# Kernel optimization log

Measured on AMD Instinct MI355X. Metric: run time of the kernel, lower is better.

## Reference

```python
import math
import jax, jax.numpy as jnp
import numpy as np

T, B, E, H = 2048, 1, 2048, 32
HD = E // H          # head_dim = 64
HALF = HD // 2       # rotary half = 32
SCALE_LENGTH = 1024


def duplicate_interleave(m):
    # [S, HALF] -> [S, HD], each column duplicated adjacently
    return jnp.repeat(m, 2, axis=-1)


def rotate_every_two(x):
    # x: [BH, S, HD]
    x1 = x[:, :, ::2]
    x2 = x[:, :, 1::2]
    return jnp.stack((-x2, x1), axis=-1).reshape(x.shape)


def apply_rotary_pos_emb(x, sin, cos, scale):
    # sin/cos/scale: [S, HALF]; x: [BH, S, HD]
    sin2 = duplicate_interleave(sin * scale)
    cos2 = duplicate_interleave(cos * scale)
    return x * cos2 + rotate_every_two(x) * sin2


def setup_inputs() -> dict:
    key = jax.random.key(0)
    ks = jax.random.split(key, 8)
    std = 0.02
    query = jax.random.normal(ks[0], (T, B, E), jnp.float32)
    key_t = jax.random.normal(ks[1], (T, B, E), jnp.float32)
    value = jax.random.normal(ks[2], (T, B, E), jnp.float32)
    Wq = jax.random.normal(ks[3], (E, E), jnp.float32) * std
    Wk = jax.random.normal(ks[4], (E, E), jnp.float32) * std
    Wv = jax.random.normal(ks[5], (E, E), jnp.float32) * std
    Wo = jax.random.normal(ks[6], (E, E), jnp.float32) * std
    bq = jnp.zeros((E,), jnp.float32)
    bk = jnp.zeros((E,), jnp.float32)
    bv = jnp.zeros((E,), jnp.float32)
    bo = jnp.zeros((E,), jnp.float32)
    # XPos-style rotary tables
    pos = jnp.arange(T, dtype=jnp.float32)
    inv_freq = 1.0 / (10000.0 ** (jnp.arange(HALF, dtype=jnp.float32) / HALF))
    ang = pos[:, None] * inv_freq[None, :]          # [T, HALF]
    sin = jnp.sin(ang)
    cos = jnp.cos(ang)
    scale_base = 512.0
    dim_scale = (jnp.arange(0, HD, 2, dtype=jnp.float32) + 0.4 * HD) / (1.4 * HD)
    xscale = dim_scale[None, :] ** (pos[:, None] / scale_base)  # [T, HALF]
    # causal additive mask
    attn_mask = jnp.where(jnp.triu(jnp.ones((T, T), bool), k=1), -1e9, 0.0).astype(jnp.float32)
    return {"query": query, "key": key_t, "value": value,
            "Wq": Wq, "bq": bq, "Wk": Wk, "bk": bk, "Wv": Wv, "bv": bv,
            "Wo": Wo, "bo": bo, "sin": sin, "cos": cos, "xscale": xscale,
            "attn_mask": attn_mask, "scale_length": SCALE_LENGTH}


def reference(query, key, value, Wq, bq, Wk, bk, Wv, bv, Wo, bo,
              sin, cos, xscale, attn_mask, scale_length):
    tgt_len, bsz, embed_dim = query.shape
    scaling = HD ** -0.5

    def proj(x, W, b):
        y = x @ W.T + b                                # [T, B, E]
        return y.reshape(tgt_len, bsz * H, HD).transpose(1, 0, 2)  # [BH, T, HD]

    q = proj(query, Wq, bq)
    k = proj(key, Wk, bk)
    v = proj(value, Wv, bv)

    # self-attention XPos rotary: k scaled by 1/xscale, q by xscale (last q_len rows)
    k = apply_rotary_pos_emb(k, sin, cos, 1.0 / xscale)
    q = apply_rotary_pos_emb(q, sin[-tgt_len:], cos[-tgt_len:], xscale[-tgt_len:])

    src_len = k.shape[1]
    if src_len > scale_length:
        pos_k = jnp.arange(src_len - tgt_len, src_len, dtype=jnp.float32)
        scale_attention = jnp.maximum(1.0, jnp.log(pos_k) / math.log(scale_length))
        q = q * scale_attention[None, :, None]

    q = q * scaling
    attn_weights = jnp.einsum('btd,bsd->bts', q, k)      # [BH, T, S]
    attn_weights = attn_weights + attn_mask[None, :, :]
    attn_weights = jax.nn.softmax(attn_weights.astype(jnp.float32), axis=-1
                                  ).astype(q.dtype)
    attn = jnp.einsum('bts,bsd->btd', attn_weights, v)   # [BH, T, HD]
    attn = attn.transpose(1, 0, 2).reshape(tgt_len, bsz, embed_dim)
    attn = attn @ Wo.T + bo
    return attn
```

## Files before the change

### kernel.cpp

```cpp
#include <hip/hip_runtime.h>
#include <hip/hip_bf16.h>
#include <math.h>

#define T_LEN 2048
#define EMB   2048
#define NH    32
#define HD    64
#define HALF  32

typedef __attribute__((ext_vector_type(8))) short short8v;
typedef __attribute__((ext_vector_type(4))) float floatx4;

__device__ inline void gload_lds16(const void* g, void* l) {
    __builtin_amdgcn_global_load_lds(
        (const __attribute__((address_space(1))) unsigned int*)g,
        (__attribute__((address_space(3))) unsigned int*)l,
        16, 0, 0);
}

__device__ inline ushort f2bf(float x) {
    union { float f; unsigned u; } c; c.f = x;
    const unsigned r = c.u + 0x7FFFu + ((c.u >> 16) & 1u);
    return (ushort)(r >> 16);
}

#define BARRIER() do { asm volatile("" ::: "memory"); \
    __builtin_amdgcn_s_barrier(); asm volatile("" ::: "memory"); } while (0)
#define VMW8() asm volatile("s_waitcnt vmcnt(8)" ::: "memory")
#define VMW0() asm volatile("s_waitcnt vmcnt(0)" ::: "memory")

__global__ __launch_bounds__(256) void conv_all(
    const float* __restrict__ s0, const float* __restrict__ s1,
    const float* __restrict__ s2, const float* __restrict__ s3,
    const float* __restrict__ s4, const float* __restrict__ s5,
    const float* __restrict__ s6, ushort* __restrict__ dst,
    const float* __restrict__ sinp, const float* __restrict__ cosp,
    const float* __restrict__ xscale,
    float2* __restrict__ qt, float2* __restrict__ kt)
{
    if (blockIdx.x >= 14336) {
        const int idx = (blockIdx.x - 14336) * 256 + threadIdx.x;
        const int t = idx >> 5;
        const float s = sinp[idx], c = cosp[idx], xs = xscale[idx];
        float sa = 1.f;
        if (t >= 2) {
            const float lv = __logf((float)t) * 0.14426950408889634f;
            sa = lv > 1.f ? lv : 1.f;
        }
        const float qs = xs * sa * 0.125f * 1.4426950408889634f;
        qt[idx] = make_float2(c * qs, s * qs);
        const float ks = 1.f / xs;
        kt[idx] = make_float2(c * ks, s * ks);
        return;
    }
    const int idx = blockIdx.x * 256 + threadIdx.x;
    const int t = idx >> 19;
    const int r = (idx & 524287) * 8;
    const float* in = t == 0 ? s0 : t == 1 ? s1 : t == 2 ? s2 : t == 3 ? s3
                    : t == 4 ? s4 : t == 5 ? s5 : s6;
    const float4 v0 = *reinterpret_cast<const float4*>(&in[r]);
    const float4 v1 = *reinterpret_cast<const float4*>(&in[r + 4]);
    ushort o[8];
    o[0] = f2bf(v0.x); o[1] = f2bf(v0.y); o[2] = f2bf(v0.z); o[3] = f2bf(v0.w);
    o[4] = f2bf(v1.x); o[5] = f2bf(v1.y); o[6] = f2bf(v1.z); o[7] = f2bf(v1.w);
    *reinterpret_cast<uint4*>(&dst[(size_t)t * 4194304 + r]) =
        *reinterpret_cast<const uint4*>(o);
}

#define QBM 256
#define QBN 256

#define STAGE_A3(tau, h, slot) do {                                            \
    const int _tc = (tau) * 64;                                                \
    _Pragma("unroll") for (int _i = 0; _i < 2; ++_i) {                         \
        gload_lds16(&Ap[(size_t)(bm + (h) * 128 + wid * 16 + _i * 8 + rl) * 2048 + _tc + csw], \
                    &lds[(slot) * 16384 + (h) * 8192 + (wid * 16 + _i * 8) * 64]); \
    } } while (0)

#define STAGE_B2(tau, h, slot) do {                                            \
    const int _tc = (tau) * 64;                                                \
    _Pragma("unroll") for (int _i = 0; _i < 2; ++_i) {                         \
        gload_lds16(&Bp[(size_t)(bn + (h) * 128 + wid * 16 + _i * 8 + rl) * 2048 + _tc + csw], \
                    &lds[49152 + (slot) * 16384 + (h) * 8192 + (wid * 16 + _i * 8) * 64]); \
    } } while (0)

#define PH(sa_, sb_, mp, VMWSTMT, PREBAR, ENDBAR, ...) do {                    \
    if ((mp) == 0) {                                                           \
        _Pragma("unroll") for (int n = 0; n < 4; ++n) {                        \
            bf[n][0] = ldB(sb_, n, 0);                                         \
            bf[n][1] = ldB(sb_, n, 1);                                         \
        }                                                                      \
    }                                                                          \
    af[0][0] = ldA(sa_, (mp) * 2, 0);     af[0][1] = ldA(sa_, (mp) * 2, 1);    \
    af[1][0] = ldA(sa_, (mp) * 2 + 1, 0); af[1][1] = ldA(sa_, (mp) * 2 + 1, 1);\
    __VA_ARGS__;                                                               \
    PREBAR;                                                                    \
    __builtin_amdgcn_s_setprio(1);                                             \
    _Pragma("unroll") for (int mm = 0; mm < 2; ++mm)                           \
    _Pragma("unroll") for (int n = 0; n < 4; ++n)                              \
    _Pragma("unroll") for (int kk = 0; kk < 2; ++kk)                           \
        acc[(mp) * 2 + mm][n] = __builtin_amdgcn_mfma_f32_16x16x32_bf16(       \
            af[mm][kk], bf[n][kk], acc[(mp) * 2 + mm][n], 0, 0, 0);            \
    __builtin_amdgcn_s_setprio(0);                                             \
    VMWSTMT;                                                                   \
    ENDBAR;                                                                    \
} while (0)

#define TILE6(sa, sb, sa2, tau2, LASTVMW) do {                                 \
    PH(sa, sb, 0, (void)0, (void)0,   (void)0,   STAGE_A3(tau2, 0, sa2));      \
    PH(sa, sb, 1, (void)0, BARRIER(), (void)0,   STAGE_A3(tau2, 1, sa2));      \
    PH(sa, sb, 2, (void)0, (void)0,   (void)0,   STAGE_B2(tau2, 0, sb));       \
    PH(sa, sb, 3, LASTVMW, (void)0,   BARRIER(), STAGE_B2(tau2, 1, sb));       \
} while (0)

__global__ __launch_bounds__(512, 2) void gemm_qkv8(
    const ushort* __restrict__ Astack,
    const ushort* __restrict__ Wstack,
    const float* __restrict__ bq, const float* __restrict__ bk,
    const float* __restrict__ bv,
    ushort* __restrict__ outQ, ushort* __restrict__ outK,
    ushort* __restrict__ outVt,
    const float2* __restrict__ qtab, const float2* __restrict__ ktab)
{
    __shared__ ushort lds[81920];
    const int tid  = threadIdx.x;
    const int lane = tid & 63;
    const int wid  = tid >> 6;

    const int b   = blockIdx.x + blockIdx.y * 24;
    const int xcd = b & 7;
    const int idx = b >> 3;
    const int bx  = xcd * 3 + (idx >> 3);
    const int by  = idx & 7;
    const int which = bx >> 3;
    const int bn  = (bx & 7) * QBN;
    const int bm  = by * QBM;
    const ushort* Ap = Astack + (size_t)which * 4194304;
    const ushort* Bp = Wstack + (size_t)which * 4194304;

    const int rl  = lane >> 3;
    const int csw = (((lane & 7) ^ ((lane >> 3) & 7)) * 8);
    const int lm  = lane & 15;
    const int lg  = lane >> 4;
    const char* ldsb = reinterpret_cast<const char*>(lds);

    auto ldA = [&](int slot, int m, int kk) -> short8v {
        const int row = m * 16 + lm;
        const int off = (slot * 16384 + (wid >> 2) * 8192) * 2 + row * 128
                      + (((kk * 4 + lg) ^ (row & 7)) * 16);
        return *reinterpret_cast<const short8v*>(ldsb + off);
    };
    auto ldB = [&](int slot, int n, int kk) -> short8v {
        const int row = (wid & 1) * 64 + n * 16 + lm;
        const int off = (49152 + slot * 16384 + ((wid & 3) >> 1) * 8192) * 2
                      + row * 128 + (((kk * 4 + lg) ^ (row & 7)) * 16);
        return *reinterpret_cast<const short8v*>(ldsb + off);
    };

    floatx4 acc[8][4] = {};
    short8v bf[4][2];
    short8v af[2][2];

    STAGE_A3(0, 0, 0); STAGE_A3(0, 1, 0);
    STAGE_B2(0, 0, 0); STAGE_B2(0, 1, 0);
    STAGE_A3(1, 0, 1); STAGE_A3(1, 1, 1);
    STAGE_B2(1, 0, 1); STAGE_B2(1, 1, 1);
    VMW8();
    BARRIER();

    for (int i = 0; i < 5; ++i) {
        const int t = 6 * i;
        TILE6(0, 0, 2, t + 2, VMW8());
        TILE6(1, 1, 0, t + 3, VMW8());
        TILE6(2, 0, 1, t + 4, VMW8());
        TILE6(0, 1, 2, t + 5, VMW8());
        TILE6(1, 0, 0, t + 6, VMW8());
        TILE6(2, 1, 1, t + 7, VMW8());
    }
    PH(0, 0, 0, (void)0, (void)0,   (void)0,   (void)0);
    PH(0, 0, 1, (void)0, (void)0,   (void)0,   (void)0);
    PH(0, 0, 2, (void)0, (void)0,   (void)0,   (void)0);
    PH(0, 0, 3, VMW0(),  (void)0,   BARRIER(), (void)0);
    PH(1, 1, 0, (void)0, (void)0, (void)0, (void)0);
    PH(1, 1, 1, (void)0, (void)0, (void)0, (void)0);
    PH(1, 1, 2, (void)0, (void)0, (void)0, (void)0);
    PH(1, 1, 3, (void)0, (void)0, (void)0, (void)0);

    const float* bias = which == 0 ? bq : which == 1 ? bk : bv;
    const float2* tbl = which == 0 ? qtab : ktab;
    #pragma unroll
    for (int m = 0; m < 8; ++m) {
        #pragma unroll
        for (int n = 0; n < 4; ++n) {
            const int col = bn + (wid & 3) * 64 + n * 16 + lm;
            const float bz = bias[col];
            const int row0 = bm + (wid >> 2) * 128 + m * 16 + lg * 4;
            if (which == 2) {
                ushort o4[4];
                #pragma unroll
                for (int j = 0; j < 4; ++j)
                    o4[j] = f2bf(acc[m][n][j] + bz);
                *reinterpret_cast<uint2*>(&outVt[(size_t)col * T_LEN + row0]) =
                    *reinterpret_cast<const uint2*>(o4);
            } else {
                ushort* O = which == 0 ? outQ : outK;
                const int p = (col & 63) >> 1;
                const bool even = (col & 1) == 0;
                #pragma unroll
                for (int j = 0; j < 4; ++j) {
                    const int row = row0 + j;
                    const float v = acc[m][n][j] + bz;
                    const float pv = __shfl_xor(v, 1);
                    const float2 cs = tbl[row * HALF + p];
                    const float outv = even ? v * cs.x - pv * cs.y
                                            : v * cs.x + pv * cs.y;
                    O[(size_t)row * EMB + col] = f2bf(outv);
                }
            }
        }
    }
}

#define GBM 128
#define GBN 128
#define GBK 64

__global__ __launch_bounds__(256) void gemm_out_sk(
    const ushort* __restrict__ A,
    const ushort* __restrict__ B,
    ushort* __restrict__ P)
{
    __shared__ ushort As[GBM * GBK];
    __shared__ ushort Bs[GBN * GBK];
    const int tid  = threadIdx.x;
    const int lane = tid & 63;
    const int wid  = tid >> 6;
    const int bm = blockIdx.y * GBM;
    const int bn = blockIdx.x * GBN;
    const int z  = blockIdx.z;
    const int wr = (wid >> 1) * 64;
    const int wc = (wid & 1) * 64;

    floatx4 acc[4][4] = {};

    const int lrow  = lane >> 3;
    const int lcolb = (lane & 7) * 8;

    for (int k0 = z * 1024; k0 < (z + 1) * 1024; k0 += GBK) {
        #pragma unroll
        for (int c = 0; c < 4; ++c) {
            const int chunk = wid * 4 + c;
            const int row = chunk * 8 + lrow;
            gload_lds16(&A[(size_t)(bm + row) * EMB + k0 + lcolb], &As[chunk * 512]);
            gload_lds16(&B[(size_t)(bn + row) * EMB + k0 + lcolb], &Bs[chunk * 512]);
        }
        __syncthreads();
        #pragma unroll
        for (int kk = 0; kk < 2; ++kk) {
            short8v a[4], b[4];
            #pragma unroll
            for (int m = 0; m < 4; ++m)
                a[m] = *reinterpret_cast<const short8v*>(
                    &As[(wr + m * 16 + (lane & 15)) * GBK + kk * 32 + (lane >> 4) * 8]);
            #pragma unroll
            for (int n = 0; n < 4; ++n)
                b[n] = *reinterpret_cast<const short8v*>(
                    &Bs[(wc + n * 16 + (lane & 15)) * GBK + kk * 32 + (lane >> 4) * 8]);
            #pragma unroll
            for (int m = 0; m < 4; ++m)
                #pragma unroll
                for (int n = 0; n < 4; ++n)
                    acc[m][n] = __builtin_amdgcn_mfma_f32_16x16x32_bf16(
                        a[m], b[n], acc[m][n], 0, 0, 0);
        }
        __syncthreads();
    }

    ushort* Pz = P + (size_t)z * 4194304;
    const int cr = (lane >> 4) * 4;
    const int cc = lane & 15;
    #pragma unroll
    for (int m = 0; m < 4; ++m) {
        #pragma unroll
        for (int n = 0; n < 4; ++n) {
            const int col = bn + wc + n * 16 + cc;
            #pragma unroll
            for (int j = 0; j < 4; ++j) {
                const int row = bm + wr + m * 16 + cr + j;
                Pz[(size_t)row * EMB + col] = f2bf(acc[m][n][j]);
            }
        }
    }
}

__global__ __launch_bounds__(256) void reduce_out(
    const ushort* __restrict__ P, const float* __restrict__ bias,
    float* __restrict__ C)
{
    const int i = (blockIdx.x * 256 + threadIdx.x) * 8;
    const uint4 pa = *reinterpret_cast<const uint4*>(&P[i]);
    const uint4 pb = *reinterpret_cast<const uint4*>(&P[4194304 + i]);
    const ushort* ua = reinterpret_cast<const ushort*>(&pa);
    const ushort* ub = reinterpret_cast<const ushort*>(&pb);
    const int cb = i & 2047;
    float o[8];
    #pragma unroll
    for (int j = 0; j < 8; ++j) {
        union { unsigned u; float f; } fa, fb;
        fa.u = (unsigned)ua[j] << 16;
        fb.u = (unsigned)ub[j] << 16;
        o[j] = fa.f + fb.f + bias[cb + j];
    }
    *reinterpret_cast<float4*>(&C[i])     = make_float4(o[0], o[1], o[2], o[3]);
    *reinterpret_cast<float4*>(&C[i + 4]) = make_float4(o[4], o[5], o[6], o[7]);
}

__global__ __launch_bounds__(256) void flash_attn_mfma(
    const ushort* __restrict__ Qb,
    const ushort* __restrict__ Kb,
    const ushort* __restrict__ Vt,
    ushort* __restrict__ Ob)
{
    __shared__ ushort Ks[2][64 * 64];
    __shared__ ushort Vs[2][64 * 64];
    __shared__ ushort Ps[4][16 * 64];

    const int h   = blockIdx.x;
    const int qb  = (T_LEN / 64 - 1) - blockIdx.y;
    const int tid = threadIdx.x;
    const int lane = tid & 63;
    const int wid  = tid >> 6;
    const int qrow_w = qb * 64 + wid * 16;
    const int lm = lane & 15;
    const int lg = lane >> 4;

    short8v qf[2];
    {
        const ushort* qp = &Qb[(size_t)(qrow_w + lm) * EMB + h * HD + lg * 8];
        qf[0] = *reinterpret_cast<const short8v*>(qp);
        qf[1] = *reinterpret_cast<const short8v*>(qp + 32);
    }

    floatx4 oacc[4] = {};
    float m = -1e30f, l = 0.f;

    const int srow = lane >> 3;
    const int schk = lane & 7;

    {
        #pragma unroll
        for (int i = 0; i < 2; ++i) {
            const int slot = wid * 2 + i;
            const int row  = slot * 8 + srow;
            const int cswz = (schk ^ (row & 7)) * 8;
            gload_lds16(&Kb[(size_t)row * EMB + h * HD + cswz], &Ks[0][slot * 512]);
            gload_lds16(&Vt[(size_t)(h * HD + row) * T_LEN + cswz], &Vs[0][slot * 512]);
        }
    }
    __syncthreads();

    for (int kb = 0; kb <= qb; ++kb) {
        const int cur = kb & 1;
        if (kb < qb) {
            const int nkb = kb + 1;
            #pragma unroll
            for (int i = 0; i < 2; ++i) {
                const int slot = wid * 2 + i;
                const int row  = slot * 8 + srow;
                const int cswz = (schk ^ (row & 7)) * 8;
                gload_lds16(&Kb[(size_t)(nkb * 64 + row) * EMB + h * HD + cswz],
                            &Ks[cur ^ 1][slot * 512]);
                gload_lds16(&Vt[(size_t)(h * HD + row) * T_LEN + nkb * 64 + cswz],
                            &Vs[cur ^ 1][slot * 512]);
            }
        }

        float sv[16];
        __builtin_amdgcn_s_setprio(1);
        #pragma unroll
        for (int t = 0; t < 4; ++t) {
            floatx4 sacc = {};
            const int srow_l = t * 16 + lm;
            const char* krow = reinterpret_cast<const char*>(Ks[cur]) + srow_l * 128;
            const int swz = (srow_l & 7) << 4;
            #pragma unroll
            for (int kk = 0; kk < 2; ++kk) {
                const int cb = (kk * 64 + lg * 16) ^ swz;
                short8v kf = *reinterpret_cast<const short8v*>(krow + cb);
                sacc = __builtin_amdgcn_mfma_f32_16x16x32_bf16(kf, qf[kk], sacc, 0, 0, 0);
            }
            sv[t * 4 + 0] = sacc[0]; sv[t * 4 + 1] = sacc[1];
            sv[t * 4 + 2] = sacc[2]; sv[t * 4 + 3] = sacc[3];
        }
        __builtin_amdgcn_s_setprio(0);

        const int qg = qrow_w + lm;
        if (kb == qb) {
            #pragma unroll
            for (int t = 0; t < 4; ++t)
                #pragma unroll
                for (int r = 0; r < 4; ++r) {
                    const int sg = kb * 64 + t * 16 + lg * 4 + r;
                    if (sg > qg) sv[t * 4 + r] = -1e30f;
                }
        }

        const float mx0 = fmaxf(fmaxf(fmaxf(sv[0], sv[1]), fmaxf(sv[2], sv[3])),
                                fmaxf(fmaxf(sv[4], sv[5]), fmaxf(sv[6], sv[7])));
        const float mx1 = fmaxf(fmaxf(fmaxf(sv[8], sv[9]), fmaxf(sv[10], sv[11])),
                                fmaxf(fmaxf(sv[12], sv[13]), fmaxf(sv[14], sv[15])));
        float mx = fmaxf(mx0, mx1);
        mx = fmaxf(mx, __shfl_xor(mx, 16));
        mx = fmaxf(mx, __shfl_xor(mx, 32));
        float corr = 1.f;
        if (!__all(mx - m <= 11.544f)) {
            const float mnew = fmaxf(m, mx);
            corr = exp2f(m - mnew);
            m = mnew;
            float corr4[4];
            #pragma unroll
            for (int r = 0; r < 4; ++r)
                corr4[r] = __shfl(corr, lg * 4 + r);
            #pragma unroll
            for (int td = 0; td < 4; ++td)
                #pragma unroll
                for (int r = 0; r < 4; ++r)
                    oacc[td][r] *= corr4[r];
        }
        float psum[8];
        unsigned pw[8];
        #pragma unroll
        for (int i = 0; i < 8; ++i) {
            const float p0 = exp2f(sv[2 * i + 0] - m);
            const float p1 = exp2f(sv[2 * i + 1] - m);
            psum[i] = p0 + p1;
            const __hip_bfloat162 h2 = __float22bfloat162_rn(make_float2(p0, p1));
            pw[i] = *reinterpret_cast<const unsigned*>(&h2);
        }
        float ps = ((psum[0] + psum[1]) + (psum[2] + psum[3]))
                 + ((psum[4] + psum[5]) + (psum[6] + psum[7]));
        ps += __shfl_xor(ps, 16);
        ps += __shfl_xor(ps, 32);
        l = l * corr + ps;

        {
            char* pbase = reinterpret_cast<char*>(&Ps[wid][0]) + lm * 128;
            const int swz = (lm & 7) << 4;
            #pragma unroll
            for (int t = 0; t < 4; ++t) {
                uint2 w;
                w.x = pw[2 * t + 0];
                w.y = pw[2 * t + 1];
                const int cb = (t * 32 + lg * 8) ^ swz;
                *reinterpret_cast<uint2*>(pbase + cb) = w;
            }
        }

        const char* pwave = reinterpret_cast<const char*>(&Ps[wid][0]);
        __builtin_amdgcn_s_setprio(1);
        #pragma unroll
        for (int kk = 0; kk < 2; ++kk) {
            const int acb = (kk * 64 + lg * 16) ^ ((lm & 7) << 4);
            short8v pa = *reinterpret_cast<const short8v*>(pwave + lm * 128 + acb);
            #pragma unroll
            for (int td = 0; td < 4; ++td) {
                const int d = td * 16 + lm;
                const int bcb = (kk * 64 + lg * 16) ^ ((d & 7) << 4);
                short8v vb = *reinterpret_cast<const short8v*>(
                    reinterpret_cast<const char*>(Vs[cur]) + d * 128 + bcb);
                oacc[td] = __builtin_amdgcn_mfma_f32_16x16x32_bf16(pa, vb, oacc[td], 0, 0, 0);
            }
        }
        __builtin_amdgcn_s_setprio(0);

        __syncthreads();
    }

    float invl[4];
    #pragma unroll
    for (int r = 0; r < 4; ++r)
        invl[r] = 1.f / __shfl(l, lg * 4 + r);
    #pragma unroll
    for (int td = 0; td < 4; ++td) {
        #pragma unroll
        for (int r = 0; r < 4; ++r) {
            const int trow = qrow_w + lg * 4 + r;
            const int col  = h * HD + td * 16 + lm;
            Ob[(size_t)trow * EMB + col] = f2bf(oacc[td][r] * invl[r]);
        }
    }
}

extern "C" void kernel_launch(void* const* d_in, const int* in_sizes, int n_in,
                              void* d_out, int out_size, void* d_ws, size_t ws_size,
                              hipStream_t stream) {
    const float* query = (const float*)d_in[0];
    const float* key   = (const float*)d_in[1];
    const float* value = (const float*)d_in[2];
    const float* Wq = (const float*)d_in[3];
    const float* bq = (const float*)d_in[4];
    const float* Wk = (const float*)d_in[5];
    const float* bk = (const float*)d_in[6];
    const float* Wv = (const float*)d_in[7];
    const float* bv = (const float*)d_in[8];
    const float* Wo = (const float*)d_in[9];
    const float* bo = (const float*)d_in[10];
    const float* sinp   = (const float*)d_in[11];
    const float* cosp   = (const float*)d_in[12];
    const float* xscale = (const float*)d_in[13];
    float* out = (float*)d_out;

    const size_t MB = 1024 * 1024;
    char* ws = (char*)d_ws;
    ushort* bWqkv = (ushort*)(ws + 0 * MB);
    ushort* bWo   = (ushort*)(ws + 24 * MB);
    ushort* bAqkv = (ushort*)(ws + 32 * MB);
    ushort* bQ  = (ushort*)(ws + 56 * MB);
    ushort* bK  = (ushort*)(ws + 64 * MB);
    ushort* bVt = (ushort*)(ws + 72 * MB);
    ushort* bAo = (ushort*)(ws + 80 * MB);
    float2* qtab = (float2*)(ws + 88 * MB);
    float2* ktab = (float2*)(ws + 88 * MB + 512 * 1024);
    ushort* Pout = (ushort*)(ws + 32 * MB);

    conv_all<<<14336 + 256, 256, 0, stream>>>(
        Wq, Wk, Wv, Wo, query, key, value, bWqkv,
        sinp, cosp, xscale, qtab, ktab);

    dim3 gQKV(24, 8);
    gemm_qkv8<<<gQKV, 512, 0, stream>>>(bAqkv, bWqkv, bq, bk, bv,
                                        bQ, bK, bVt, qtab, ktab);

    dim3 gFlash(NH, T_LEN / 64);
    flash_attn_mfma<<<gFlash, 256, 0, stream>>>(bQ, bK, bVt, bAo);

    dim3 gOut(EMB / GBN, T_LEN / GBM, 2);
    gemm_out_sk<<<gOut, 256, 0, stream>>>(bAo, bWo, Pout);
    reduce_out<<<T_LEN * EMB / (256 * 8), 256, 0, stream>>>(Pout, bo, out);
}
```

Measured before the change: 167.6 us.

## Fuse fp32-to-bf16 activation conversion into the QKV GEMM A-tile staging

The separate conversion pass for query/key/value activations is removed. The QKV GEMM now loads fp32 A tiles into registers, packs them to bf16 and writes them to swizzled LDS itself, with a reworked software pipeline and waitcnt schedule. This saves writing and re-reading 24MB of bf16 activations. In exchange it doubles the GEMM's global A traffic, raises register pressure, and the A loads no longer use direct-to-LDS transfers.

Result: slower. 268.2 us (+60.1%).

```diff
diff --git a/kernel.cpp b/kernel.cpp
--- a/kernel.cpp
+++ b/kernel.cpp
@@ -24,22 +24,30 @@
     return (ushort)(r >> 16);
 }
 
+__device__ inline unsigned pk2bf(float a, float b) {
+    __hip_bfloat162 h2 = __float22bfloat162_rn(make_float2(a, b));
+    return *reinterpret_cast<unsigned*>(&h2);
+}
+
 #define BARRIER() do { asm volatile("" ::: "memory"); \
     __builtin_amdgcn_s_barrier(); asm volatile("" ::: "memory"); } while (0)
-#define VMW8() asm volatile("s_waitcnt vmcnt(8)" ::: "memory")
-#define VMW0() asm volatile("s_waitcnt vmcnt(0)" ::: "memory")
+#define VMW16() asm volatile("s_waitcnt vmcnt(16)" ::: "memory")
+#define VMW12() asm volatile("s_waitcnt vmcnt(12)" ::: "memory")
+#define VMW8()  asm volatile("s_waitcnt vmcnt(8)"  ::: "memory")
+#define VMW4()  asm volatile("s_waitcnt vmcnt(4)"  ::: "memory")
+#define VMW0()  asm volatile("s_waitcnt vmcnt(0)"  ::: "memory")
+#define LGKM0() asm volatile("s_waitcnt lgkmcnt(0)" ::: "memory")
 
 __global__ __launch_bounds__(256) void conv_all(
     const float* __restrict__ s0, const float* __restrict__ s1,
     const float* __restrict__ s2, const float* __restrict__ s3,
-    const float* __restrict__ s4, const float* __restrict__ s5,
-    const float* __restrict__ s6, ushort* __restrict__ dst,
+    ushort* __restrict__ dst,
     const float* __restrict__ sinp, const float* __restrict__ cosp,
     const float* __restrict__ xscale,
     float2* __restrict__ qt, float2* __restrict__ kt)
 {
-    if (blockIdx.x >= 14336) {
-        const int idx = (blockIdx.x - 14336) * 256 + threadIdx.x;
+    if (blockIdx.x >= 8192) {
+        const int idx = (blockIdx.x - 8192) * 256 + threadIdx.x;
         const int t = idx >> 5;
         const float s = sinp[idx], c = cosp[idx], xs = xscale[idx];
         float sa = 1.f;
@@ -56,8 +64,7 @@
     const int idx = blockIdx.x * 256 + threadIdx.x;
     const int t = idx >> 19;
     const int r = (idx & 524287) * 8;
-    const float* in = t == 0 ? s0 : t == 1 ? s1 : t == 2 ? s2 : t == 3 ? s3
-                    : t == 4 ? s4 : t == 5 ? s5 : s6;
+    const float* in = t == 0 ? s0 : t == 1 ? s1 : t == 2 ? s2 : s3;
     const float4 v0 = *reinterpret_cast<const float4*>(&in[r]);
     const float4 v1 = *reinterpret_cast<const float4*>(&in[r + 4]);
     ushort o[8];
@@ -70,13 +77,6 @@
 #define QBM 256
 #define QBN 256
 
-#define STAGE_A3(tau, h, slot) do {                                            \
-    const int _tc = (tau) * 64;                                                \
-    _Pragma("unroll") for (int _i = 0; _i < 2; ++_i) {                         \
-        gload_lds16(&Ap[(size_t)(bm + (h) * 128 + wid * 16 + _i * 8 + rl) * 2048 + _tc + csw], \
-                    &lds[(slot) * 16384 + (h) * 8192 + (wid * 16 + _i * 8) * 64]); \
-    } } while (0)
-
 #define STAGE_B2(tau, h, slot) do {                                            \
     const int _tc = (tau) * 64;                                                \
     _Pragma("unroll") for (int _i = 0; _i < 2; ++_i) {                         \
@@ -84,17 +84,37 @@
                     &lds[49152 + (slot) * 16384 + (h) * 8192 + (wid * 16 + _i * 8) * 64]); \
     } } while (0)
 
-#define PH(sa_, sb_, mp, VMWSTMT, PREBAR, ENDBAR, ...) do {                    \
-    if ((mp) == 0) {                                                           \
-        _Pragma("unroll") for (int n = 0; n < 4; ++n) {                        \
-            bf[n][0] = ldB(sb_, n, 0);                                         \
-            bf[n][1] = ldB(sb_, n, 1);                                         \
-        }                                                                      \
-    }                                                                          \
+#define LOAD_A(tau, h) do {                                                    \
+    _Pragma("unroll") for (int _i = 0; _i < 2; ++_i) {                         \
+        const float* _s = &Af[(size_t)(bm + (h) * 128 + wid * 16 + _i * 8 + rl) * 2048 \
+                              + (tau) * 64 + (lane & 7) * 8];                  \
+        arA[h][_i] = *reinterpret_cast<const float4*>(_s);                     \
+        arB[h][_i] = *reinterpret_cast<const float4*>(_s + 4);                 \
+    } } while (0)
+
+#define WRITE_A(h, slot) do {                                                  \
+    _Pragma("unroll") for (int _i = 0; _i < 2; ++_i) {                         \
+        uint4 _v;                                                              \
+        _v.x = pk2bf(arA[h][_i].x, arA[h][_i].y);                              \
+        _v.y = pk2bf(arA[h][_i].z, arA[h][_i].w);                              \
+        _v.z = pk2bf(arB[h][_i].x, arB[h][_i].y);                              \
+        _v.w = pk2bf(arB[h][_i].z, arB[h][_i].w);                              \
+        *reinterpret_cast<uint4*>(ldsw + (slot) * 32768 + (h) * 16384          \
+            + (wid * 16 + _i * 8 + rl) * 128 + (((lane & 7) ^ rl) * 16)) = _v; \
+    } } while (0)
+
+#define RDB(sb_) do {                                                          \
+    _Pragma("unroll") for (int n = 0; n < 4; ++n) {                            \
+        bf[n][0] = ldB(sb_, n, 0);                                             \
+        bf[n][1] = ldB(sb_, n, 1);                                             \
+    } } while (0)
+
+#define RDA(sa_, mp) do {                                                      \
     af[0][0] = ldA(sa_, (mp) * 2, 0);     af[0][1] = ldA(sa_, (mp) * 2, 1);    \
     af[1][0] = ldA(sa_, (mp) * 2 + 1, 0); af[1][1] = ldA(sa_, (mp) * 2 + 1, 1);\
-    __VA_ARGS__;                                                               \
-    PREBAR;                                                                    \
+    } while (0)
+
+#define MFMA(mp) do {                                                          \
     __builtin_amdgcn_s_setprio(1);                                             \
     _Pragma("unroll") for (int mm = 0; mm < 2; ++mm)                           \
     _Pragma("unroll") for (int n = 0; n < 4; ++n)                              \
@@ -102,19 +122,19 @@
         acc[(mp) * 2 + mm][n] = __builtin_amdgcn_mfma_f32_16x16x32_bf16(       \
             af[mm][kk], bf[n][kk], acc[(mp) * 2 + mm][n], 0, 0, 0);            \
     __builtin_amdgcn_s_setprio(0);                                             \
-    VMWSTMT;                                                                   \
-    ENDBAR;                                                                    \
 } while (0)
 
-#define TILE6(sa, sb, sa2, tau2, LASTVMW) do {                                 \
-    PH(sa, sb, 0, (void)0, (void)0,   (void)0,   STAGE_A3(tau2, 0, sa2));      \
-    PH(sa, sb, 1, (void)0, BARRIER(), (void)0,   STAGE_A3(tau2, 1, sa2));      \
-    PH(sa, sb, 2, (void)0, (void)0,   (void)0,   STAGE_B2(tau2, 0, sb));       \
-    PH(sa, sb, 3, LASTVMW, (void)0,   BARRIER(), STAGE_B2(tau2, 1, sb));       \
+#define TILE6F(saR, saW, sb, tau2) do {                                        \
+    RDB(sb); RDA(saR, 0); VMW8(); WRITE_A(0, saW); LOAD_A(tau2, 0); MFMA(0);   \
+    RDA(saR, 1); VMW8(); WRITE_A(1, saW); LOAD_A(tau2, 1); BARRIER(); MFMA(1); \
+    RDA(saR, 2); STAGE_B2(tau2, 0, sb); MFMA(2);                               \
+    RDA(saR, 3); STAGE_B2(tau2, 1, sb); MFMA(3); VMW12(); LGKM0(); BARRIER();  \
 } while (0)
 
 __global__ __launch_bounds__(512, 2) void gemm_qkv8(
-    const ushort* __restrict__ Astack,
+    const float* __restrict__ Aq,
+    const float* __restrict__ Ak,
+    const float* __restrict__ Av,
     const ushort* __restrict__ Wstack,
     const float* __restrict__ bq, const float* __restrict__ bk,
     const float* __restrict__ bv,
@@ -135,7 +155,7 @@
     const int which = bx >> 3;
     const int bn  = (bx & 7) * QBN;
     const int bm  = by * QBM;
-    const ushort* Ap = Astack + (size_t)which * 4194304;
+    const float* Af  = which == 0 ? Aq : which == 1 ? Ak : Av;
     const ushort* Bp = Wstack + (size_t)which * 4194304;
 
     const int rl  = lane >> 3;
@@ -143,6 +163,7 @@
     const int lm  = lane & 15;
     const int lg  = lane >> 4;
     const char* ldsb = reinterpret_cast<const char*>(lds);
+    char* ldsw = reinterpret_cast<char*>(lds);
 
     auto ldA = [&](int slot, int m, int kk) -> short8v {
         const int row = m * 16 + lm;
@@ -160,31 +181,35 @@
     floatx4 acc[8][4] = {};
     short8v bf[4][2];
     short8v af[2][2];
-
-    STAGE_A3(0, 0, 0); STAGE_A3(0, 1, 0);
+    float4 arA[2][2], arB[2][2];
+
+    LOAD_A(0, 0); LOAD_A(0, 1);
     STAGE_B2(0, 0, 0); STAGE_B2(0, 1, 0);
-    STAGE_A3(1, 0, 1); STAGE_A3(1, 1, 1);
+    VMW16();
+    WRITE_A(0, 0); WRITE_A(1, 0);
+    LOAD_A(1, 0); LOAD_A(1, 1);
     STAGE_B2(1, 0, 1); STAGE_B2(1, 1, 1);
-    VMW8();
+    VMW12();
+    LGKM0();
     BARRIER();
 
     for (int i = 0; i < 5; ++i) {
         const int t = 6 * i;
-        TILE6(0, 0, 2, t + 2, VMW8());
-        TILE6(1, 1, 0, t + 3, VMW8());
-        TILE6(2, 0, 1, t + 4, VMW8());
-        TILE6(0, 1, 2, t + 5, VMW8());
-        TILE6(1, 0, 0, t + 6, VMW8());
-        TILE6(2, 1, 1, t + 7, VMW8());
-    }
-    PH(0, 0, 0, (void)0, (void)0,   (void)0,   (void)0);
-    PH(0, 0, 1, (void)0, (void)0,   (void)0,   (void)0);
-    PH(0, 0, 2, (void)0, (void)0,   (void)0,   (void)0);
-    PH(0, 0, 3, VMW0(),  (void)0,   BARRIER(), (void)0);
-    PH(1, 1, 0, (void)0, (void)0, (void)0, (void)0);
-    PH(1, 1, 1, (void)0, (void)0, (void)0, (void)0);
-    PH(1, 1, 2, (void)0, (void)0, (void)0, (void)0);
-    PH(1, 1, 3, (void)0, (void)0, (void)0, (void)0);
+        TILE6F(0, 1, 0, t + 2);
+        TILE6F(1, 2, 1, t + 3);
+        TILE6F(2, 0, 0, t + 4);
+        TILE6F(0, 1, 1, t + 5);
+        TILE6F(1, 2, 0, t + 6);
+        TILE6F(2, 1 == 1 ? 0 : 0, 1, t + 7);
+    }
+    RDB(0); RDA(0, 0); VMW8(); WRITE_A(0, 1); MFMA(0);
+    RDA(0, 1); VMW4(); WRITE_A(1, 1); BARRIER(); MFMA(1);
+    RDA(0, 2); MFMA(2);
+    RDA(0, 3); MFMA(3); VMW0(); LGKM0(); BARRIER();
+    RDB(1); RDA(1, 0); MFMA(0);
+    RDA(1, 1); MFMA(1);
+    RDA(1, 2); MFMA(2);
+    RDA(1, 3); MFMA(3);
 
     const float* bias = which == 0 ? bq : which == 1 ? bk : bv;
     const float2* tbl = which == 0 ? qtab : ktab;
@@ -434,8 +459,7 @@
             const float p0 = exp2f(sv[2 * i + 0] - m);
             const float p1 = exp2f(sv[2 * i + 1] - m);
             psum[i] = p0 + p1;
-            const __hip_bfloat162 h2 = __float22bfloat162_rn(make_float2(p0, p1));
-            pw[i] = *reinterpret_cast<const unsigned*>(&h2);
+            pw[i] = pk2bf(p0, p1);
         }
         float ps = ((psum[0] + psum[1]) + (psum[2] + psum[3]))
                  + ((psum[4] + psum[5]) + (psum[6] + psum[7]));
@@ -513,23 +537,21 @@
     const size_t MB = 1024 * 1024;
     char* ws = (char*)d_ws;
     ushort* bWqkv = (ushort*)(ws + 0 * MB);
-    ushort* bWo   = (ushort*)(ws + 24 * MB);
-    ushort* bAqkv = (ushort*)(ws + 32 * MB);
     ushort* bQ  = (ushort*)(ws + 56 * MB);
     ushort* bK  = (ushort*)(ws + 64 * MB);
     ushort* bVt = (ushort*)(ws + 72 * MB);
     ushort* bAo = (ushort*)(ws + 80 * MB);
     float2* qtab = (float2*)(ws + 88 * MB);
     float2* ktab = (float2*)(ws + 88 * MB + 512 * 1024);
+    ushort* bWo  = (ushort*)(ws + 24 * MB);
     ushort* Pout = (ushort*)(ws + 32 * MB);
 
-    conv_all<<<14336 + 256, 256, 0, stream>>>(
-        Wq, Wk, Wv, Wo, query, key, value, bWqkv,
-        sinp, cosp, xscale, qtab, ktab);
+    conv_all<<<8192 + 256, 256, 0, stream>>>(
+        Wq, Wk, Wv, Wo, bWqkv, sinp, cosp, xscale, qtab, ktab);
 
     dim3 gQKV(24, 8);
-    gemm_qkv8<<<gQKV, 512, 0, stream>>>(bAqkv, bWqkv, bq, bk, bv,
-                                        bQ, bK, bVt, qtab, ktab);
+    gemm_qkv8<<<gQKV, 512, 0, stream>>>(query, key, value, bWqkv,
+                                        bq, bk, bv, bQ, bK, bVt, qtab, ktab);
 
     dim3 gFlash(NH, T_LEN / 64);
     flash_attn_mfma<<<gFlash, 256, 0, stream>>>(bQ, bK, bVt, bAo);
```
